# Kernel optimization log

Hardware: AMD Instinct MI355X
Metric: run time of the kernel (lower is better)

The kernel has to match this reference:

```python
import jax, jax.numpy as jnp
import numpy as np

B, S, D, H, C, E, V = 8, 2048, 1024, 512, 256, 64, 64


def setup_inputs() -> dict:
    key = jax.random.key(0)
    ks = jax.random.split(key, 40)
    ri = lambda i, hi: jax.random.randint(ks[i], (B, S), 0, hi).astype(jnp.int32)
    p = lambda i, shape: (jax.random.normal(ks[i], shape, jnp.float32) * 0.02)
    inp = {
        'h_x': jax.random.normal(ks[0], (B, S, D), jnp.float32),
        'h_y': jax.random.normal(ks[1], (B, S, D), jnp.float32),
        'x_mask': jnp.ones((B, S), jnp.int32),
        'y_mask': jnp.ones((B, S), jnp.int32),
        'src_token_dense_mask': ri(2, 2), 'src_token_sparse_mask': ri(3, 2),
        'src_token_inarc_type': ri(4, V), 'src_token_arc_head': ri(5, S),
        'src_token_depth': ri(6, 16), 'src_word_inarc_type': ri(7, V),
        'src_word_inarc_type_mask': ri(8, 2),
        'tgt_token_dense_mask': ri(9, 2), 'tgt_token_sparse_mask': ri(10, 2),
        'tgt_token_inarc_type': ri(11, V), 'tgt_token_arc_head': ri(12, S),
        'tgt_token_depth': ri(13, 16), 'tgt_word_inarc_type': ri(14, V),
        'tgt_word_inarc_type_mask': ri(15, 2),
        # src MLP [D->H->C], tgt MLP [D->H->C]
        'W1s': p(16, (D, H)), 'b1s': jnp.zeros((H,), jnp.float32),
        'W2s': p(17, (H, C)), 'b2s': jnp.zeros((C,), jnp.float32),
        'W1t': p(18, (D, H)), 'b1t': jnp.zeros((H,), jnp.float32),
        'W2t': p(19, (H, C)), 'b2t': jnp.zeros((C,), jnp.float32),
        # inarc edge embedding + GeneralConv params
        'emb': p(20, (V, E)),
        'W_msg': p(21, (C, C)), 'b_msg': jnp.zeros((C,), jnp.float32),
        'W_edge': p(22, (E, C)),
        'att': p(23, (C,)),
        'W_self': p(24, (C, C)), 'b_self': jnp.zeros((C,), jnp.float32),
        # axis_feature MLP [C->C]
        'Wf': p(25, (C, C)), 'bf': jnp.zeros((C,), jnp.float32),
    }
    return inp


def _mlp(h, W1, b1, W2, b2):
    return jax.nn.leaky_relu(h @ W1 + b1) @ W2 + b2


def _graph_side(h, dense_m, sparse_m, arc_head, word_type, word_mask,
                W1, b1, W2, b2, emb, W_msg, b_msg, W_edge, att, W_self, b_self, Wf, bf):
    Bn, Sn, _ = h.shape
    x = _mlp(h, W1, b1, W2, b2)                      # [B,S,C]
    N = Bn * Sn
    Cn = x.shape[-1]
    xg = x.reshape(N, Cn)                            # debatch -> nodes
    off = (jnp.arange(Bn, dtype=jnp.int32) * Sn)[:, None]
    src = (arc_head + off).reshape(N)                # global head index per token
    dst = jnp.arange(N, dtype=jnp.int32)             # one in-edge per token
    valid = (sparse_m * dense_m).reshape(N).astype(x.dtype)
    ef = emb[(word_type * word_mask).reshape(N)]     # [N,E] edge embeddings
    # GeneralConv: directed message with edge features + additive attention
    m = xg[src] @ W_msg + b_msg + ef @ W_edge        # [N,C] messages
    hd = xg @ W_msg + b_msg                          # dst-side term for attention
    logit = jax.nn.leaky_relu(((m + hd) * att).sum(-1))
    logit = jnp.where(valid > 0, logit, -1e9)
    emax = jax.ops.segment_max(logit, dst, num_segments=N)
    ex = jnp.exp(logit - emax[dst]) * valid
    den = jax.ops.segment_sum(ex, dst, num_segments=N)
    alpha = ex / (den[dst] + 1e-16)                  # softmax per destination node
    agg = jax.ops.segment_sum(m * alpha[:, None], dst, num_segments=N)
    out = xg @ W_self + b_self + agg                 # skip_linear
    out = out / jnp.maximum(jnp.linalg.norm(out, axis=-1, keepdims=True), 1e-12)
    r = out.reshape(Bn, Sn, Cn).mean(axis=1, keepdims=True)  # FeatureRepr mean
    return r @ Wf + bf                               # [B,1,C]


def reference(h_x, x_mask, src_token_dense_mask, src_token_sparse_mask,
              src_token_inarc_type, src_token_arc_head, src_token_depth,
              src_word_inarc_type, src_word_inarc_type_mask,
              h_y, y_mask, tgt_token_dense_mask, tgt_token_sparse_mask,
              tgt_token_inarc_type, tgt_token_arc_head, tgt_token_depth,
              tgt_word_inarc_type, tgt_word_inarc_type_mask,
              W1s, b1s, W2s, b2s, W1t, b1t, W2t, b2t,
              emb, W_msg, b_msg, W_edge, att, W_self, b_self, Wf, bf):
    src_repr = _graph_side(h_x, src_token_dense_mask, src_token_sparse_mask,
                           src_token_arc_head, src_word_inarc_type, src_word_inarc_type_mask,
                           W1s, b1s, W2s, b2s, emb, W_msg, b_msg, W_edge, att,
                           W_self, b_self, Wf, bf)
    tgt_repr = _graph_side(h_y, tgt_token_dense_mask, tgt_token_sparse_mask,
                           tgt_token_arc_head, tgt_word_inarc_type, tgt_word_inarc_type_mask,
                           W1t, b1t, W2t, b2t, emb, W_msg, b_msg, W_edge, att,
                           W_self, b_self, Wf, bf)
    return (src_repr, tgt_repr)
```

## Files before the change

kernel.cpp:

```cpp
#include <hip/hip_runtime.h>
#include <stdint.h>

#define SEQ   2048
#define NNODE 16384

typedef short  short8  __attribute__((ext_vector_type(8)));
typedef float  float4v __attribute__((ext_vector_type(4)));
typedef unsigned short u16;
typedef unsigned short u16x8 __attribute__((ext_vector_type(8)));
typedef short  short4v __attribute__((ext_vector_type(4)));

__device__ __forceinline__ float b2f(u16 u) {
    union { unsigned int i; float f; } x; x.i = ((unsigned int)u) << 16; return x.f;
}
__device__ __forceinline__ u16 f2b(float f) {
    union { float f; unsigned int i; } x; x.f = f;
    unsigned int u = x.i;
    unsigned int r = (u + 0x7fffu + ((u >> 16) & 1u)) >> 16;
    return (u16)r;
}

__device__ __forceinline__ void gld16(const void* g, void* l) {
    __builtin_amdgcn_global_load_lds(
        (const __attribute__((address_space(1))) void*)g,
        (__attribute__((address_space(3))) void*)l, 16, 0, 0);
}

struct GemmP {
    const void*  A[2];
    const u16*   B[2];
    const float* bias[2];
    u16*         out[2];
};

template <int NB>
__device__ __forceinline__ void mfma4n(const short8* af, const short8* bq,
                                       float4v (*acc)[8]) {
#pragma unroll
    for (int mi = 0; mi < 4; ++mi)
#pragma unroll
        for (int ni = 0; ni < 4; ++ni)
            acc[mi][NB + ni] = __builtin_amdgcn_mfma_f32_16x16x32_bf16(
                af[mi], bq[ni], acc[mi][NB + ni], 0, 0, 0);
}

#define TILE_BODY(AC, BC, KN, AG, BG, ACV, PL, PC)                            \
    {                                                                         \
        short8 bq[4], af[4];                                                  \
        _Pragma("unroll") for (int ni = 0; ni < 4; ++ni)                      \
            bq[ni] = *(const short8*)((BC) + boff + ni * 512);                \
        _Pragma("unroll") for (int mi = 0; mi < 4; ++mi)                      \
            af[mi] = *(const short8*)((AC) + aoff + mi * 512);                \
        if constexpr (AF32) prefA32(KN, PL); else stageA16(KN, AG);           \
        __builtin_amdgcn_s_barrier();                                         \
        __builtin_amdgcn_s_setprio(1);                                        \
        mfma4n<0>(af, bq, acc);                                               \
        __builtin_amdgcn_s_setprio(0);                                        \
        __builtin_amdgcn_s_barrier();                                         \
        _Pragma("unroll") for (int ni = 0; ni < 4; ++ni)                      \
            bq[ni] = *(const short8*)((BC) + boff + (4 + ni) * 512);          \
        stageB(KN, BG);                                                       \
        if constexpr (AF32) {                                                 \
            cvtWrite(PC, ACV);                                                \
            asm volatile("s_waitcnt lgkmcnt(0)" ::: "memory");                \
            asm volatile("s_waitcnt vmcnt(8)" ::: "memory");                  \
        } else {                                                              \
            asm volatile("s_waitcnt vmcnt(6)" ::: "memory");                  \
        }                                                                     \
        __builtin_amdgcn_s_barrier();                                         \
        __builtin_amdgcn_s_setprio(1);                                        \
        mfma4n<4>(af, bq, acc);                                               \
        __builtin_amdgcn_s_setprio(0);                                        \
        __builtin_amdgcn_s_barrier();                                         \
    }

template <int ACT, int AF32>
__global__ __launch_bounds__(256, 2) void gemm8_k(GemmP p, int M, int N, int K) {
    __shared__ __align__(16) u16 smem[36864];

    const int z = blockIdx.z;
    const u16*   __restrict__ Bg   = p.B[z];
    const float* __restrict__ bias = p.bias[z];
    const u16*   __restrict__ A16  = (const u16*)p.A[z];
    const float* __restrict__ A32  = (const float*)p.A[z];

    const int mt  = blockIdx.x * 128;
    const int nt  = blockIdx.y * 256;
    const int tid = threadIdx.x;
    const int l   = tid & 63;
    const int w   = tid >> 6;
    const int wm  = (w >> 1) * 64;
    const int wn  = (w & 1) * 128;
    const int lr  = l & 15;
    const int lk  = l >> 4;
    (void)M;

    float4v acc[4][8] = {};
    float4v paA[4], paB[4];

    const int rm0 = tid >> 2;
    const int cc0 = tid & 3;
    const int gc0 = cc0 ^ (rm0 & 3) ^ ((rm0 >> 2) & 3);

    u16* const As0 = smem;
    u16* const Bs0 = smem + 12288;

    auto stageA16 = [&](int k0, u16* dst) {
        gld16(A16 + (size_t)(mt + rm0) * K + k0 + gc0 * 8, dst + tid * 8);
        gld16(A16 + (size_t)(mt + rm0 + 64) * K + k0 + gc0 * 8,
              dst + (tid + 256) * 8);
    };
    auto stageB = [&](int k0, u16* dst) {
#pragma unroll
        for (int it = 0; it < 4; ++it)
            gld16(Bg + (size_t)(nt + rm0 + 64 * it) * K + k0 + gc0 * 8,
                  dst + (size_t)(tid + 256 * it) * 8);
    };
    auto prefA32 = [&](int k0, float4v* pa) {
        const float* s0 = A32 + (size_t)(mt + rm0) * K + k0 + gc0 * 8;
        const float* s1 = A32 + (size_t)(mt + rm0 + 64) * K + k0 + gc0 * 8;
        pa[0] = *(const float4v*)s0; pa[1] = *(const float4v*)(s0 + 4);
        pa[2] = *(const float4v*)s1; pa[3] = *(const float4v*)(s1 + 4);
    };
    auto cvtWrite = [&](const float4v* pa, u16* dst) {
        u16x8 r0, r1;
        r0[0]=f2b(pa[0][0]); r0[1]=f2b(pa[0][1]); r0[2]=f2b(pa[0][2]); r0[3]=f2b(pa[0][3]);
        r0[4]=f2b(pa[1][0]); r0[5]=f2b(pa[1][1]); r0[6]=f2b(pa[1][2]); r0[7]=f2b(pa[1][3]);
        r1[0]=f2b(pa[2][0]); r1[1]=f2b(pa[2][1]); r1[2]=f2b(pa[2][2]); r1[3]=f2b(pa[2][3]);
        r1[4]=f2b(pa[3][0]); r1[5]=f2b(pa[3][1]); r1[6]=f2b(pa[3][2]); r1[7]=f2b(pa[3][3]);
        *(u16x8*)(dst + tid * 8) = r0;
        *(u16x8*)(dst + (tid + 256) * 8) = r1;
    };

    const int fsl  = lk ^ (lr & 3) ^ ((lr >> 2) & 3);
    const int aoff = (wm + lr) * 32 + fsl * 8;
    const int boff = (wn + lr) * 32 + fsl * 8;

    const int KT = K >> 5;

    if constexpr (AF32) {
        float4v p0[4];
        prefA32(0, p0);
        stageB(0, Bs0);
        prefA32(32, paB);
        stageB(32, Bs0 + 8192);
        cvtWrite(p0, As0);
        asm volatile("s_waitcnt vmcnt(8)" ::: "memory");
        asm volatile("s_waitcnt lgkmcnt(0)" ::: "memory");
    } else {
        stageA16(0, As0);          stageB(0, Bs0);
        stageA16(32, As0 + 4096);  stageB(32, Bs0 + 8192);
        asm volatile("s_waitcnt vmcnt(6)" ::: "memory");
    }
    __builtin_amdgcn_s_barrier();

    int sc = 0;
    for (int kt = 0; kt < KT; kt += 2) {
        const int sc1 = (sc == 2) ? 0 : sc + 1;
        const int sc2 = (sc1 == 2) ? 0 : sc1 + 1;
        u16* Ae = As0 + sc  * 4096;  u16* Be = Bs0 + sc  * 8192;
        u16* Ao = As0 + sc1 * 4096;  u16* Bo = Bs0 + sc1 * 8192;
        u16* A2 = As0 + sc2 * 4096;  u16* B2 = Bs0 + sc2 * 8192;
        const int k2 = (kt + 2 < KT) ? (kt + 2) << 5 : 0;
        const int k3 = (kt + 3 < KT) ? (kt + 3) << 5 : 0;
        TILE_BODY(Ae, Be, k2, A2, B2, Ao, paA, paB)
        TILE_BODY(Ao, Bo, k3, Ae, Be, A2, paB, paA)
        sc = sc2;
    }

    __syncthreads();

    const int er0 = lk * 4;
    float bvv[8];
#pragma unroll
    for (int ni = 0; ni < 8; ++ni) bvv[ni] = bias[nt + wn + ni * 16 + lr];
#pragma unroll
    for (int mi = 0; mi < 4; ++mi)
#pragma unroll
        for (int ni = 0; ni < 8; ++ni) {
            const int lc = wn + ni * 16 + lr;
#pragma unroll
            for (int r = 0; r < 4; ++r) {
                float v = acc[mi][ni][r] + bvv[ni];
                if (ACT) v = v > 0.f ? v : 0.01f * v;
                smem[(size_t)(wm + mi * 16 + er0 + r) * 264 + lc] = f2b(v);
            }
        }
    __syncthreads();
#pragma unroll
    for (int it = 0; it < 16; ++it) {
        const int id  = it * 256 + tid;
        const int row = id >> 5, colc = id & 31;
        u16x8 vv = *(const u16x8*)(smem + (size_t)row * 264 + colc * 8);
        *(u16x8*)(p.out[z] + (size_t)(mt + row) * N + nt + colc * 8) = vv;
    }
}

struct TP { const float* src[6]; u16* dst[6]; int K[6]; int N[6]; };

__global__ __launch_bounds__(256) void transpose_k(TP t) {
    __shared__ float tile[64][65];
    const int m = blockIdx.y;
    const int K = t.K[m], N = t.N[m];
    const int tn = N >> 6;
    const int ntiles = (K >> 6) * tn;
    const int bid = blockIdx.x;
    if (bid >= ntiles) return;
    const int k0 = (bid / tn) * 64, n0 = (bid % tn) * 64;
    const int tid = threadIdx.x;
#pragma unroll
    for (int pass = 0; pass < 4; ++pass) {
        int kk = pass * 16 + (tid >> 4);
        int nn = (tid & 15) * 4;
        float4v v = *(const float4v*)(t.src[m] + (size_t)(k0 + kk) * N + n0 + nn);
        tile[kk][nn + 0] = v[0]; tile[kk][nn + 1] = v[1];
        tile[kk][nn + 2] = v[2]; tile[kk][nn + 3] = v[3];
    }
    __syncthreads();
    const int n = tid >> 2, kc = (tid & 3) * 16;
    u16x8 a, b;
#pragma unroll
    for (int j = 0; j < 8; ++j) {
        a[j] = f2b(tile[kc + j][n]);
        b[j] = f2b(tile[kc + 8 + j][n]);
    }
    u16* d = t.dst[m] + (size_t)(n0 + n) * K + k0 + kc;
    *(u16x8*)d = a;
    *(u16x8*)(d + 8) = b;
}

__global__ void ew_k(const float* emb, const float* W_edge, float* EW) {
    const int t = blockIdx.x, c = threadIdx.x;
    float p0 = 0.f, p1 = 0.f, p2 = 0.f, p3 = 0.f;
    for (int e = 0; e < 64; e += 4) {
        p0 += emb[t * 64 + e + 0] * W_edge[(e + 0) * 256 + c];
        p1 += emb[t * 64 + e + 1] * W_edge[(e + 1) * 256 + c];
        p2 += emb[t * 64 + e + 2] * W_edge[(e + 2) * 256 + c];
        p3 += emb[t * 64 + e + 3] * W_edge[(e + 3) * 256 + c];
    }
    EW[t * 256 + c] = (p0 + p1) + (p2 + p3);
}

struct WmP { const float* W2[2]; const float* Wmsg; const float* Wself;
             float* W23[2]; };

__global__ __launch_bounds__(512) void wmul_k(WmP q) {
    __shared__ float w2[16][256];
    const int side = blockIdx.y;
    const int k0 = blockIdx.x * 16;
    const int n = threadIdx.x;
    const float* __restrict__ W2 = q.W2[side];
    for (int i = threadIdx.x; i < 4096; i += 512)
        w2[i >> 8][i & 255] = W2[(size_t)(k0 + (i >> 8)) * 256 + (i & 255)];
    __syncthreads();
    const float* __restrict__ Wc = (n < 256) ? q.Wmsg : q.Wself;
    const int nn = n & 255;
    float acc[16] = {};
    for (int c = 0; c < 256; c += 4) {
        const float wc0 = Wc[(c + 0) * 256 + nn];
        const float wc1 = Wc[(c + 1) * 256 + nn];
        const float wc2 = Wc[(c + 2) * 256 + nn];
        const float wc3 = Wc[(c + 3) * 256 + nn];
#pragma unroll
        for (int kk = 0; kk < 16; ++kk)
            acc[kk] += w2[kk][c] * wc0 + w2[kk][c + 1] * wc1 +
                       w2[kk][c + 2] * wc2 + w2[kk][c + 3] * wc3;
    }
    for (int kk = 0; kk < 16; ++kk)
        q.W23[side][(size_t)(k0 + kk) * 512 + n] = acc[kk];
}

struct B23WP { const float* b2[2]; const float* bmsg; const float* bself;
               const float* Wmsg; const float* Wself; float* b23; };

__global__ void b23w_k(B23WP q) {
    const int side = blockIdx.x;
    const int n = threadIdx.x;
    const float* __restrict__ W = (n < 256) ? q.Wmsg : q.Wself;
    const int nn = n & 255;
    const float* __restrict__ b2 = q.b2[side];
    float p[8] = {};
    for (int c = 0; c < 256; c += 8) {
#pragma unroll
        for (int j = 0; j < 8; ++j)
            p[j] += b2[c + j] * W[(c + j) * 256 + nn];
    }
    float s = (n < 256) ? q.bmsg[nn] : q.bself[nn];
    s += ((p[0] + p[1]) + (p[2] + p[3])) + ((p[4] + p[5]) + (p[6] + p[7]));
    q.b23[side * 512 + n] = s;
}

struct EpiP {
    const u16* xcat[2];
    const int* den[2]; const int* spa[2]; const int* arc[2];
    const int* wty[2]; const int* wma[2];
    const float* EW; float* racc;
};

__global__ __launch_bounds__(256) void epi_k(EpiP p) {
    __shared__ float part[4][256];
    const int bx    = blockIdx.x;
    const int side  = bx >> 9;
    const int local = bx & 511;
    const int base  = local * 32;
    const int b     = base >> 11;
    const int tid   = threadIdx.x;
    const int w = tid >> 6, l = tid & 63;

    const u16* __restrict__ xcat = p.xcat[side];

    float4v acc = {};
    for (int j = 0; j < 8; ++j) {
        const int i     = base + w * 8 + j;
        const int valid = p.den[side][i] * p.spa[side][i];
        const int srcn  = p.arc[side][i] + (i >> 11) * SEQ;
        const int t     = p.wty[side][i] * p.wma[side][i];
        short4v xs = *(const short4v*)(xcat + (size_t)i * 512 + 256 + l * 4);
        short4v xm = *(const short4v*)(xcat + (size_t)srcn * 512 + l * 4);
        float4v ew = *(const float4v*)(p.EW + (size_t)t * 256 + l * 4);
        const float vm = valid ? 1.f : 0.f;
        float4v v;
        v[0] = b2f((u16)xs[0]) + vm * (b2f((u16)xm[0]) + ew[0]);
        v[1] = b2f((u16)xs[1]) + vm * (b2f((u16)xm[1]) + ew[1]);
        v[2] = b2f((u16)xs[2]) + vm * (b2f((u16)xm[2]) + ew[2]);
        v[3] = b2f((u16)xs[3]) + vm * (b2f((u16)xm[3]) + ew[3]);
        float ss = v[0]*v[0] + v[1]*v[1] + v[2]*v[2] + v[3]*v[3];
        for (int m = 32; m >= 1; m >>= 1) ss += __shfl_xor(ss, m, 64);
        const float rn = 1.f / fmaxf(sqrtf(ss), 1e-12f);
        acc[0] += v[0] * rn; acc[1] += v[1] * rn;
        acc[2] += v[2] * rn; acc[3] += v[3] * rn;
    }
    part[w][l * 4 + 0] = acc[0];
    part[w][l * 4 + 1] = acc[1];
    part[w][l * 4 + 2] = acc[2];
    part[w][l * 4 + 3] = acc[3];
    __syncthreads();
    const float s = part[0][tid] + part[1][tid] + part[2][tid] + part[3][tid];
    atomicAdd(p.racc + ((size_t)side * 8 + b) * 256 + tid, s);
}

__global__ void fin_k(const float* racc, const float* Wf, const float* bfv,
                      float* out) {
    __shared__ float r[256];
    const int bid = blockIdx.x;
    const int tid = threadIdx.x;
    r[tid] = racc[bid * 256 + tid] * (1.f / 2048.f);
    __syncthreads();
    float s = bfv[tid];
    for (int k = 0; k < 256; ++k)
        s += r[k] * Wf[k * 256 + tid];
    out[bid * 256 + tid] = s;
}

extern "C" void kernel_launch(void* const* d_in, const int* in_sizes, int n_in,
                              void* d_out, int out_size, void* d_ws, size_t ws_size,
                              hipStream_t stream) {
    const float* h[2]   = {(const float*)d_in[0],  (const float*)d_in[1]};
    const int* den[2]   = {(const int*)d_in[4],  (const int*)d_in[11]};
    const int* spa[2]   = {(const int*)d_in[5],  (const int*)d_in[12]};
    const int* arc[2]   = {(const int*)d_in[7],  (const int*)d_in[14]};
    const int* wty[2]   = {(const int*)d_in[9],  (const int*)d_in[16]};
    const int* wma[2]   = {(const int*)d_in[10], (const int*)d_in[17]};
    const float* W1[2]  = {(const float*)d_in[18], (const float*)d_in[22]};
    const float* b1[2]  = {(const float*)d_in[19], (const float*)d_in[23]};
    const float* W2[2]  = {(const float*)d_in[20], (const float*)d_in[24]};
    const float* b2[2]  = {(const float*)d_in[21], (const float*)d_in[25]};
    const float* emb    = (const float*)d_in[26];
    const float* Wmsg   = (const float*)d_in[27];
    const float* bmsg   = (const float*)d_in[28];
    const float* Wedge  = (const float*)d_in[29];
    const float* Wself  = (const float*)d_in[31];
    const float* bself  = (const float*)d_in[32];
    const float* Wf     = (const float*)d_in[33];
    const float* bf_    = (const float*)d_in[34];

    char* ws = (char*)d_ws;
    size_t off = 0;
    auto alloc = [&](size_t bytes) -> void* {
        void* pp = ws + off; off += (bytes + 255) & ~(size_t)255; return pp;
    };
    u16*   x1    = (u16*)  alloc(2ull * NNODE * 512 * 2);
    u16*   xcat  = (u16*)  alloc(2ull * NNODE * 512 * 2);
    u16*   W1T   = (u16*)  alloc(2ull * 512 * 1024 * 2);
    float* W23   = (float*)alloc(2ull * 512 * 512 * 4);
    u16*   W23T  = (u16*)  alloc(2ull * 512 * 512 * 2);
    float* EW    = (float*)alloc(64 * 256 * 4);
    float* b23   = (float*)alloc(2 * 512 * 4);
    float* racc  = (float*)alloc(2 * 8 * 256 * 4);

    TP tp = {};
    tp.src[0] = W1[0]; tp.dst[0] = W1T;              tp.K[0] = 1024; tp.N[0] = 512;
    tp.src[1] = W1[1]; tp.dst[1] = W1T + 512 * 1024; tp.K[1] = 1024; tp.N[1] = 512;
    hipLaunchKernelGGL(transpose_k, dim3(128, 2), dim3(256), 0, stream, tp);
    hipLaunchKernelGGL(ew_k, dim3(64), dim3(256), 0, stream, emb, Wedge, EW);

    WmP wq;
    wq.W2[0] = W2[0]; wq.W2[1] = W2[1];
    wq.Wmsg = Wmsg; wq.Wself = Wself;
    wq.W23[0] = W23; wq.W23[1] = W23 + 512 * 512;
    hipLaunchKernelGGL(wmul_k, dim3(32, 2), dim3(512), 0, stream, wq);

    TP tp2 = {};
    tp2.src[0] = W23;            tp2.dst[0] = W23T;            tp2.K[0] = 512; tp2.N[0] = 512;
    tp2.src[1] = W23 + 512*512;  tp2.dst[1] = W23T + 512*512;  tp2.K[1] = 512; tp2.N[1] = 512;
    hipLaunchKernelGGL(transpose_k, dim3(64, 2), dim3(256), 0, stream, tp2);

    B23WP bq;
    bq.b2[0] = b2[0]; bq.b2[1] = b2[1];
    bq.bmsg = bmsg; bq.bself = bself;
    bq.Wmsg = Wmsg; bq.Wself = Wself;
    bq.b23 = b23;
    hipLaunchKernelGGL(b23w_k, dim3(2), dim3(512), 0, stream, bq);
    hipMemsetAsync(racc, 0, 2 * 8 * 256 * 4, stream);

    GemmP g1 = {};
    g1.A[0] = h[0];  g1.A[1] = h[1];
    g1.B[0] = W1T;   g1.B[1] = W1T + 512 * 1024;
    g1.bias[0] = b1[0]; g1.bias[1] = b1[1];
    g1.out[0] = x1;  g1.out[1] = x1 + (size_t)NNODE * 512;
    hipLaunchKernelGGL((gemm8_k<1, 1>), dim3(128, 2, 2), dim3(256), 0, stream,
                       g1, NNODE, 512, 1024);

    GemmP g23 = {};
    g23.A[0] = x1;   g23.A[1] = x1 + (size_t)NNODE * 512;
    g23.B[0] = W23T; g23.B[1] = W23T + 512 * 512;
    g23.bias[0] = b23; g23.bias[1] = b23 + 512;
    g23.out[0] = xcat; g23.out[1] = xcat + (size_t)NNODE * 512;
    hipLaunchKernelGGL((gemm8_k<0, 0>), dim3(128, 2, 2), dim3(256), 0, stream,
                       g23, NNODE, 512, 512);

    EpiP ep;
    ep.xcat[0] = xcat; ep.xcat[1] = xcat + (size_t)NNODE * 512;
    for (int s = 0; s < 2; ++s) {
        ep.den[s] = den[s]; ep.spa[s] = spa[s]; ep.arc[s] = arc[s];
        ep.wty[s] = wty[s]; ep.wma[s] = wma[s];
    }
    ep.EW = EW; ep.racc = racc;
    hipLaunchKernelGGL(epi_k, dim3(1024), dim3(256), 0, stream, ep);

    hipLaunchKernelGGL(fin_k, dim3(16), dim3(256), 0, stream,
                       racc, Wf, bf_, (float*)d_out);
}
```

Before: 349.2 us.

## Restructure bf16 GEMM to 256x128 tiles with BK=64 and a separate input conversion

Replaces the 128x256, BK=32 GEMM, which converted fp32 A to bf16 in registers, with a 512-thread kernel. The new kernel uses 256x128 tiles, a 64-wide K step with XOR-swizzled LDS, and three-stage async global-to-LDS staging for both operands. The fp32 hidden states are now converted to bf16 by a standalone kernel first, so the first GEMM can load A directly into LDS. The intent is better MFMA pipelining and simpler staging. The cost is an extra full read/write pass over the inputs and a much larger LDS footprint per block, which may limit occupancy.

```diff
diff --git a/kernel.cpp b/kernel.cpp
--- a/kernel.cpp
+++ b/kernel.cpp
@@ -27,172 +27,135 @@
 }
 
 struct GemmP {
-    const void*  A[2];
+    const u16*   A[2];
     const u16*   B[2];
     const float* bias[2];
     u16*         out[2];
 };
 
-template <int NB>
-__device__ __forceinline__ void mfma4n(const short8* af, const short8* bq,
-                                       float4v (*acc)[8]) {
-#pragma unroll
-    for (int mi = 0; mi < 4; ++mi)
-#pragma unroll
-        for (int ni = 0; ni < 4; ++ni)
-            acc[mi][NB + ni] = __builtin_amdgcn_mfma_f32_16x16x32_bf16(
-                af[mi], bq[ni], acc[mi][NB + ni], 0, 0, 0);
-}
-
-#define TILE_BODY(AC, BC, KN, AG, BG, ACV, PL, PC)                            \
+#define PHASE(ASL, BSL, KH, STAGE, DO_VM)                                     \
     {                                                                         \
-        short8 bq[4], af[4];                                                  \
+        short8 af[4], bq[4];                                                  \
+        _Pragma("unroll") for (int mi = 0; mi < 4; ++mi)                      \
+            af[mi] = *(const short8*)((ASL) +                                 \
+                (size_t)(wm * 64 + mi * 16 + lr) * 64 +                       \
+                (((KH) * 4 + lk) ^ (lr & 7)) * 8);                            \
         _Pragma("unroll") for (int ni = 0; ni < 4; ++ni)                      \
-            bq[ni] = *(const short8*)((BC) + boff + ni * 512);                \
+            bq[ni] = *(const short8*)((BSL) +                                 \
+                (size_t)(wn * 64 + ni * 16 + lr) * 64 +                       \
+                (((KH) * 4 + lk) ^ (lr & 7)) * 8);                            \
+        STAGE;                                                                \
+        if (DO_VM) asm volatile("s_waitcnt vmcnt(6)" ::: "memory");           \
+        __builtin_amdgcn_s_barrier();                                         \
+        asm volatile("s_waitcnt lgkmcnt(0)" ::: "memory");                    \
+        __builtin_amdgcn_s_setprio(1);                                        \
         _Pragma("unroll") for (int mi = 0; mi < 4; ++mi)                      \
-            af[mi] = *(const short8*)((AC) + aoff + mi * 512);                \
-        if constexpr (AF32) prefA32(KN, PL); else stageA16(KN, AG);           \
-        __builtin_amdgcn_s_barrier();                                         \
-        __builtin_amdgcn_s_setprio(1);                                        \
-        mfma4n<0>(af, bq, acc);                                               \
+            _Pragma("unroll") for (int ni = 0; ni < 4; ++ni)                  \
+                acc[mi][ni] = __builtin_amdgcn_mfma_f32_16x16x32_bf16(        \
+                    af[mi], bq[ni], acc[mi][ni], 0, 0, 0);                    \
         __builtin_amdgcn_s_setprio(0);                                        \
         __builtin_amdgcn_s_barrier();                                         \
-        _Pragma("unroll") for (int ni = 0; ni < 4; ++ni)                      \
-            bq[ni] = *(const short8*)((BC) + boff + (4 + ni) * 512);          \
-        stageB(KN, BG);                                                       \
-        if constexpr (AF32) {                                                 \
-            cvtWrite(PC, ACV);                                                \
-            asm volatile("s_waitcnt lgkmcnt(0)" ::: "memory");                \
-            asm volatile("s_waitcnt vmcnt(8)" ::: "memory");                  \
-        } else {                                                              \
-            asm volatile("s_waitcnt vmcnt(6)" ::: "memory");                  \
-        }                                                                     \
-        __builtin_amdgcn_s_barrier();                                         \
-        __builtin_amdgcn_s_setprio(1);                                        \
-        mfma4n<4>(af, bq, acc);                                               \
-        __builtin_amdgcn_s_setprio(0);                                        \
-        __builtin_amdgcn_s_barrier();                                         \
-    }
-
-template <int ACT, int AF32>
-__global__ __launch_bounds__(256, 2) void gemm8_k(GemmP p, int M, int N, int K) {
-    __shared__ __align__(16) u16 smem[36864];
+    }
+
+template <int ACT>
+__global__ __launch_bounds__(512, 2) void gemmt_k(GemmP p, int M, int N, int K) {
+    __shared__ __align__(16) u16 smem[73728];
 
     const int z = blockIdx.z;
+    const u16*   __restrict__ Ag   = p.A[z];
     const u16*   __restrict__ Bg   = p.B[z];
     const float* __restrict__ bias = p.bias[z];
-    const u16*   __restrict__ A16  = (const u16*)p.A[z];
-    const float* __restrict__ A32  = (const float*)p.A[z];
-
-    const int mt  = blockIdx.x * 128;
-    const int nt  = blockIdx.y * 256;
+
+    const int mt  = blockIdx.x * 256;
+    const int nt  = blockIdx.y * 128;
     const int tid = threadIdx.x;
     const int l   = tid & 63;
     const int w   = tid >> 6;
-    const int wm  = (w >> 1) * 64;
-    const int wn  = (w & 1) * 128;
+    const int wm  = w >> 1;
+    const int wn  = w & 1;
     const int lr  = l & 15;
     const int lk  = l >> 4;
     (void)M;
 
-    float4v acc[4][8] = {};
-    float4v paA[4], paB[4];
-
-    const int rm0 = tid >> 2;
-    const int cc0 = tid & 3;
-    const int gc0 = cc0 ^ (rm0 & 3) ^ ((rm0 >> 2) & 3);
+    float4v acc[4][4] = {};
+
+    const int srow   = tid >> 3;
+    const int gchunk = (tid & 7) ^ (srow & 7);
 
     u16* const As0 = smem;
-    u16* const Bs0 = smem + 12288;
-
-    auto stageA16 = [&](int k0, u16* dst) {
-        gld16(A16 + (size_t)(mt + rm0) * K + k0 + gc0 * 8, dst + tid * 8);
-        gld16(A16 + (size_t)(mt + rm0 + 64) * K + k0 + gc0 * 8,
-              dst + (tid + 256) * 8);
+    u16* const Bs0 = smem + 49152;
+
+    auto stageA = [&](int k0, u16* dst) {
+#pragma unroll
+        for (int i = 0; i < 4; ++i)
+            gld16(Ag + (size_t)(mt + srow + 64 * i) * K + k0 + gchunk * 8,
+                  dst + (size_t)(tid + 512 * i) * 8);
     };
     auto stageB = [&](int k0, u16* dst) {
 #pragma unroll
-        for (int it = 0; it < 4; ++it)
-            gld16(Bg + (size_t)(nt + rm0 + 64 * it) * K + k0 + gc0 * 8,
-                  dst + (size_t)(tid + 256 * it) * 8);
+        for (int i = 0; i < 2; ++i)
+            gld16(Bg + (size_t)(nt + srow + 64 * i) * K + k0 + gchunk * 8,
+                  dst + (size_t)(tid + 512 * i) * 8);
     };
-    auto prefA32 = [&](int k0, float4v* pa) {
-        const float* s0 = A32 + (size_t)(mt + rm0) * K + k0 + gc0 * 8;
-        const float* s1 = A32 + (size_t)(mt + rm0 + 64) * K + k0 + gc0 * 8;
-        pa[0] = *(const float4v*)s0; pa[1] = *(const float4v*)(s0 + 4);
-        pa[2] = *(const float4v*)s1; pa[3] = *(const float4v*)(s1 + 4);
-    };
-    auto cvtWrite = [&](const float4v* pa, u16* dst) {
-        u16x8 r0, r1;
-        r0[0]=f2b(pa[0][0]); r0[1]=f2b(pa[0][1]); r0[2]=f2b(pa[0][2]); r0[3]=f2b(pa[0][3]);
-        r0[4]=f2b(pa[1][0]); r0[5]=f2b(pa[1][1]); r0[6]=f2b(pa[1][2]); r0[7]=f2b(pa[1][3]);
-        r1[0]=f2b(pa[2][0]); r1[1]=f2b(pa[2][1]); r1[2]=f2b(pa[2][2]); r1[3]=f2b(pa[2][3]);
-        r1[4]=f2b(pa[3][0]); r1[5]=f2b(pa[3][1]); r1[6]=f2b(pa[3][2]); r1[7]=f2b(pa[3][3]);
-        *(u16x8*)(dst + tid * 8) = r0;
-        *(u16x8*)(dst + (tid + 256) * 8) = r1;
-    };
-
-    const int fsl  = lk ^ (lr & 3) ^ ((lr >> 2) & 3);
-    const int aoff = (wm + lr) * 32 + fsl * 8;
-    const int boff = (wn + lr) * 32 + fsl * 8;
-
-    const int KT = K >> 5;
-
-    if constexpr (AF32) {
-        float4v p0[4];
-        prefA32(0, p0);
-        stageB(0, Bs0);
-        prefA32(32, paB);
-        stageB(32, Bs0 + 8192);
-        cvtWrite(p0, As0);
-        asm volatile("s_waitcnt vmcnt(8)" ::: "memory");
-        asm volatile("s_waitcnt lgkmcnt(0)" ::: "memory");
-    } else {
-        stageA16(0, As0);          stageB(0, Bs0);
-        stageA16(32, As0 + 4096);  stageB(32, Bs0 + 8192);
-        asm volatile("s_waitcnt vmcnt(6)" ::: "memory");
-    }
+
+    const int NT = K >> 6;
+
+    stageA(0, As0);       stageB(0, Bs0);
+    stageA(64, As0 + 16384); stageB(64, Bs0 + 8192);
+    asm volatile("s_waitcnt vmcnt(6)" ::: "memory");
     __builtin_amdgcn_s_barrier();
 
     int sc = 0;
-    for (int kt = 0; kt < KT; kt += 2) {
-        const int sc1 = (sc == 2) ? 0 : sc + 1;
-        const int sc2 = (sc1 == 2) ? 0 : sc1 + 1;
-        u16* Ae = As0 + sc  * 4096;  u16* Be = Bs0 + sc  * 8192;
-        u16* Ao = As0 + sc1 * 4096;  u16* Bo = Bs0 + sc1 * 8192;
-        u16* A2 = As0 + sc2 * 4096;  u16* B2 = Bs0 + sc2 * 8192;
-        const int k2 = (kt + 2 < KT) ? (kt + 2) << 5 : 0;
-        const int k3 = (kt + 3 < KT) ? (kt + 3) << 5 : 0;
-        TILE_BODY(Ae, Be, k2, A2, B2, Ao, paA, paB)
-        TILE_BODY(Ao, Bo, k3, Ae, Be, A2, paB, paA)
-        sc = sc2;
+    for (int T = 0; T < NT; ++T) {
+        const int sc2 = (sc >= 1) ? sc - 1 : 2;
+        u16* Ac = As0 + sc  * 16384;  u16* Bc = Bs0 + sc  * 8192;
+        u16* A2 = As0 + sc2 * 16384;  u16* B2 = Bs0 + sc2 * 8192;
+        const int k2 = (T + 2 < NT) ? (T + 2) << 6 : 0;
+        PHASE(Ac, Bc, 0, stageA(k2, A2), 0)
+        PHASE(Ac, Bc, 1, stageB(k2, B2), 1)
+        sc = (sc == 2) ? 0 : sc + 1;
     }
 
     __syncthreads();
 
     const int er0 = lk * 4;
-    float bvv[8];
-#pragma unroll
-    for (int ni = 0; ni < 8; ++ni) bvv[ni] = bias[nt + wn + ni * 16 + lr];
+    float bvv[4];
+#pragma unroll
+    for (int ni = 0; ni < 4; ++ni) bvv[ni] = bias[nt + wn * 64 + ni * 16 + lr];
 #pragma unroll
     for (int mi = 0; mi < 4; ++mi)
 #pragma unroll
-        for (int ni = 0; ni < 8; ++ni) {
-            const int lc = wn + ni * 16 + lr;
+        for (int ni = 0; ni < 4; ++ni) {
+            const int lc = wn * 64 + ni * 16 + lr;
 #pragma unroll
             for (int r = 0; r < 4; ++r) {
                 float v = acc[mi][ni][r] + bvv[ni];
                 if (ACT) v = v > 0.f ? v : 0.01f * v;
-                smem[(size_t)(wm + mi * 16 + er0 + r) * 264 + lc] = f2b(v);
+                smem[(size_t)(wm * 64 + mi * 16 + er0 + r) * 136 + lc] = f2b(v);
             }
         }
     __syncthreads();
 #pragma unroll
-    for (int it = 0; it < 16; ++it) {
-        const int id  = it * 256 + tid;
-        const int row = id >> 5, colc = id & 31;
-        u16x8 vv = *(const u16x8*)(smem + (size_t)row * 264 + colc * 8);
+    for (int it = 0; it < 8; ++it) {
+        const int id  = it * 512 + tid;
+        const int row = id >> 4, colc = id & 15;
+        u16x8 vv = *(const u16x8*)(smem + (size_t)row * 136 + colc * 8);
         *(u16x8*)(p.out[z] + (size_t)(mt + row) * N + nt + colc * 8) = vv;
+    }
+}
+
+struct CvtP { const float* src[2]; u16* dst[2]; };
+
+__global__ __launch_bounds__(256) void cvt_k(CvtP q, int n8) {
+    const int side = blockIdx.y;
+    const float4v* __restrict__ s = (const float4v*)q.src[side];
+    u16* __restrict__ d = q.dst[side];
+    for (int i = blockIdx.x * 256 + threadIdx.x; i < n8; i += gridDim.x * 256) {
+        float4v a = s[2 * i], b = s[2 * i + 1];
+        u16x8 r;
+        r[0] = f2b(a[0]); r[1] = f2b(a[1]); r[2] = f2b(a[2]); r[3] = f2b(a[3]);
+        r[4] = f2b(b[0]); r[5] = f2b(b[1]); r[6] = f2b(b[2]); r[7] = f2b(b[3]);
+        *(u16x8*)(d + (size_t)i * 8) = r;
     }
 }
 
@@ -380,13 +343,20 @@
         void* pp = ws + off; off += (bytes + 255) & ~(size_t)255; return pp;
     };
     u16*   x1    = (u16*)  alloc(2ull * NNODE * 512 * 2);
-    u16*   xcat  = (u16*)  alloc(2ull * NNODE * 512 * 2);
+    u16*   hb    = (u16*)  alloc(2ull * NNODE * 1024 * 2);
+    u16*   xcat  = hb;
     u16*   W1T   = (u16*)  alloc(2ull * 512 * 1024 * 2);
     float* W23   = (float*)alloc(2ull * 512 * 512 * 4);
     u16*   W23T  = (u16*)  alloc(2ull * 512 * 512 * 2);
     float* EW    = (float*)alloc(64 * 256 * 4);
     float* b23   = (float*)alloc(2 * 512 * 4);
     float* racc  = (float*)alloc(2 * 8 * 256 * 4);
+
+    CvtP cq;
+    cq.src[0] = h[0]; cq.src[1] = h[1];
+    cq.dst[0] = hb;   cq.dst[1] = hb + (size_t)NNODE * 1024;
+    hipLaunchKernelGGL(cvt_k, dim3(2048, 2), dim3(256), 0, stream,
+                       cq, NNODE * 1024 / 8);
 
     TP tp = {};
     tp.src[0] = W1[0]; tp.dst[0] = W1T;              tp.K[0] = 1024; tp.N[0] = 512;
@@ -414,11 +384,11 @@
     hipMemsetAsync(racc, 0, 2 * 8 * 256 * 4, stream);
 
     GemmP g1 = {};
-    g1.A[0] = h[0];  g1.A[1] = h[1];
-    g1.B[0] = W1T;   g1.B[1] = W1T + 512 * 1024;
+    g1.A[0] = hb;  g1.A[1] = hb + (size_t)NNODE * 1024;
+    g1.B[0] = W1T; g1.B[1] = W1T + 512 * 1024;
     g1.bias[0] = b1[0]; g1.bias[1] = b1[1];
-    g1.out[0] = x1;  g1.out[1] = x1 + (size_t)NNODE * 512;
-    hipLaunchKernelGGL((gemm8_k<1, 1>), dim3(128, 2, 2), dim3(256), 0, stream,
+    g1.out[0] = x1; g1.out[1] = x1 + (size_t)NNODE * 512;
+    hipLaunchKernelGGL((gemmt_k<1>), dim3(64, 4, 2), dim3(512), 0, stream,
                        g1, NNODE, 512, 1024);
 
     GemmP g23 = {};
@@ -426,7 +396,7 @@
     g23.B[0] = W23T; g23.B[1] = W23T + 512 * 512;
     g23.bias[0] = b23; g23.bias[1] = b23 + 512;
     g23.out[0] = xcat; g23.out[1] = xcat + (size_t)NNODE * 512;
-    hipLaunchKernelGGL((gemm8_k<0, 0>), dim3(128, 2, 2), dim3(256), 0, stream,
+    hipLaunchKernelGGL((gemmt_k<0>), dim3(64, 4, 2), dim3(512), 0, stream,
                        g23, NNODE, 512, 512);
 
     EpiP ep;
```

Result: slower. 368.5 us (+5.5%).
